# Optimization experiments

Hardware: AMD Instinct MI355X
Metric: run time of the kernel (lower is better)

## Reference

```python
import jax, jax.numpy as jnp
import numpy as np

EPS = 1e-5  # torch BatchNorm2d default


def _conv(x, w, padding):
    return jax.lax.conv_general_dilated(
        x, w, window_strides=(1, 1),
        padding=[(padding, padding), (padding, padding)],
        dimension_numbers=("NCHW", "OIHW", "NCHW"))


def _bn(x, gamma, beta):
    # training-mode batchnorm (biased variance), matching nn.BatchNorm2d forward
    mu = x.mean(axis=(0, 2, 3), keepdims=True)
    var = x.var(axis=(0, 2, 3), keepdims=True)
    xn = (x - mu) * jax.lax.rsqrt(var + EPS)
    return gamma[None, :, None, None] * xn + beta[None, :, None, None]


def _ste(x):
    # forward: sign(x); backward: pass gradient where |x| <= 1 (STE)
    m = (jnp.abs(x) <= 1.0).astype(x.dtype)
    s = jax.lax.stop_gradient(jnp.sign(x))
    return s + m * x - jax.lax.stop_gradient(m * x)


def _binconv(x, w, alpha, padding=1):
    # XNOR-style: sign both operands, full-precision conv, scale by alpha
    return _conv(jnp.sign(x), jnp.sign(w), padding) * alpha


def _maxpool2(x):
    return jax.lax.reduce_window(x, -jnp.inf, jax.lax.max,
                                 (1, 1, 2, 2), (1, 1, 2, 2), "VALID")


def setup_inputs() -> dict:
    key = jax.random.key(0)
    ks = jax.random.split(key, 8)

    def kaiming(k, shape):
        fan_out = shape[0] * shape[2] * shape[3]
        std = np.sqrt(2.0 / fan_out)
        return jax.random.normal(k, shape, dtype=jnp.float32) * std

    return {
        "x": jax.random.normal(ks[0], (128, 1, 128, 128), dtype=jnp.float32),
        # first conv (full precision) 1->32, k=3, pad=1
        "w1": kaiming(ks[1], (32, 1, 3, 3)),
        "b1": jnp.zeros((32,), jnp.float32),
        "g1": jnp.ones((32,), jnp.float32),
        "beta1": jnp.zeros((32,), jnp.float32),
        # BinaryConv2d 32->32
        "w2": kaiming(ks[2], (32, 32, 3, 3)),
        "a2": jnp.ones((1,), jnp.float32),
        "g2": jnp.ones((32,), jnp.float32),
        "beta2": jnp.zeros((32,), jnp.float32),
        # BinaryConv2d 32->64
        "w3": kaiming(ks[3], (64, 32, 3, 3)),
        "a3": jnp.ones((1,), jnp.float32),
        "g3": jnp.ones((64,), jnp.float32),
        "beta3": jnp.zeros((64,), jnp.float32),
        # BinaryConv2d 64->128
        "w4": kaiming(ks[4], (128, 64, 3, 3)),
        "a4": jnp.ones((1,), jnp.float32),
        # classifier 128->10
        "wf": jax.random.normal(ks[5], (10, 128), dtype=jnp.float32) * (1.0 / np.sqrt(128.0)),
        "bf": jnp.zeros((10,), jnp.float32),
    }


def reference(x, w1, b1, g1, beta1, w2, a2, g2, beta2, w3, a3, g3, beta3, w4, a4, wf, bf):
    h = _conv(x, w1, padding=1) + b1[None, :, None, None]   # [N,32,128,128]
    h = _bn(h, g1, beta1)
    h = _ste(h)
    h = _binconv(h, w2, a2)                                 # [N,32,128,128]
    h = _maxpool2(h)                                        # [N,32,64,64]
    h = _bn(h, g2, beta2)
    h = _ste(h)
    h = _binconv(h, w3, a3)                                 # [N,64,64,64]
    h = _maxpool2(h)                                        # [N,64,32,32]
    h = _bn(h, g3, beta3)
    h = _ste(h)
    h = _binconv(h, w4, a4)                                 # [N,128,32,32]
    h = h.mean(axis=(2, 3))                                 # AdaptiveAvgPool2d(1) -> [N,128]
    return h @ wf.T + bf                                    # [N,10]
```

## Files before the change

kernel.cpp:

```cpp
#include <hip/hip_runtime.h>
#include <stdint.h>
#include <limits.h>

constexpr int NB = 128;

__global__ void pack_weights_kernel(const float* __restrict__ w, uint32_t* __restrict__ out,
                                    int OC, int ICW)
{
    int idx = blockIdx.x * blockDim.x + threadIdx.x;
    int total = OC * 9 * ICW;
    if (idx >= total) return;
    int iw = idx % ICW;
    int t  = (idx / ICW) % 9;
    int oc = idx / (9 * ICW);
    int IC = ICW * 32;
    uint32_t word = 0;
    for (int b = 0; b < 32; ++b) {
        float wv = w[(size_t)(oc * IC + (iw * 32 + b)) * 9 + t];
        word |= (wv > 0.f ? 1u : 0u) << b;
    }
    out[idx] = word;
}

__device__ __forceinline__ void conv1_load9(const float* __restrict__ x, int p, float* xv)
{
    int n = p >> 14;
    int y = (p >> 7) & 127;
    int c = p & 127;
    const float* xn = x + (size_t)n * 16384;
    #pragma unroll
    for (int ky = 0; ky < 3; ++ky)
    #pragma unroll
    for (int kx = 0; kx < 3; ++kx) {
        int yy = y + ky - 1, cc = c + kx - 1;
        float v = 0.f;
        if (yy >= 0 && yy < 128 && cc >= 0 && cc < 128) v = xn[yy * 128 + cc];
        xv[ky * 3 + kx] = v;
    }
}

__global__ __launch_bounds__(256) void xcorr_kernel(const float* __restrict__ x,
                                                    float* __restrict__ partials)
{
    __shared__ float wbuf[4][64];
    int tid = threadIdx.x;
    float s[9], c[45];
    #pragma unroll
    for (int t = 0; t < 9; ++t) s[t] = 0.f;
    #pragma unroll
    for (int q = 0; q < 45; ++q) c[q] = 0.f;

    int base = blockIdx.x * 256 + tid;
    #pragma unroll 4
    for (int k = 0; k < 16; ++k) {
        float xv[9];
        conv1_load9(x, base + k * 131072, xv);
        #pragma unroll
        for (int t = 0; t < 9; ++t) {
            s[t] += xv[t];
            #pragma unroll
            for (int u = t; u < 9; ++u) {
                int q = t * (19 - t) / 2 + (u - t);
                c[q] = fmaf(xv[t], xv[u], c[q]);
            }
        }
    }
    #pragma unroll
    for (int t = 0; t < 9; ++t) {
        float a = s[t];
        #pragma unroll
        for (int off = 32; off >= 1; off >>= 1) a += __shfl_xor(a, off, 64);
        s[t] = a;
    }
    #pragma unroll
    for (int q = 0; q < 45; ++q) {
        float a = c[q];
        #pragma unroll
        for (int off = 32; off >= 1; off >>= 1) a += __shfl_xor(a, off, 64);
        c[q] = a;
    }
    int lane = tid & 63, wv = tid >> 6;
    if (lane == 0) {
        #pragma unroll
        for (int t = 0; t < 9; ++t) wbuf[wv][t] = s[t];
        #pragma unroll
        for (int q = 0; q < 45; ++q) wbuf[wv][9 + q] = c[q];
    }
    __syncthreads();
    if (tid < 54)
        partials[blockIdx.x * 64 + tid] =
            (wbuf[0][tid] + wbuf[1][tid]) + (wbuf[2][tid] + wbuf[3][tid]);
}

__global__ void compute_ss1_kernel(const double* __restrict__ dsums,
                                   const float* __restrict__ w1, const float* __restrict__ b1,
                                   const float* __restrict__ g1, const float* __restrict__ be1,
                                   float* __restrict__ ss)
{
    __shared__ double S[9], C[45];
    int tid = threadIdx.x;
    if (tid < 9) S[tid] = dsums[tid];
    else if (tid < 54) C[tid - 9] = dsums[tid];
    __syncthreads();
    if (tid >= 32) return;
    double b = (double)b1[tid];
    double w[9];
    #pragma unroll
    for (int t = 0; t < 9; ++t) w[t] = (double)w1[tid * 9 + t];
    double Sdot = 0.0, Q = 0.0;
    #pragma unroll
    for (int t = 0; t < 9; ++t) {
        Sdot += w[t] * S[t];
        #pragma unroll
        for (int u = t; u < 9; ++u) {
            int q = t * (19 - t) / 2 + (u - t);
            double term = w[t] * w[u] * C[q];
            Q += (u == t) ? term : 2.0 * term;
        }
    }
    const double N = 2097152.0;
    double mu  = Sdot / N + b;
    double ex2 = (Q + 2.0 * b * Sdot) / N + b * b;
    float var = (float)(ex2 - mu * mu);
    float A = g1[tid] * (1.f / sqrtf(var + 1e-5f));
    ss[tid] = A;
    ss[32 + tid] = be1[tid] - (float)mu * A;
}

__global__ __launch_bounds__(256) void conv1_pack_kernel(
    const float* __restrict__ x, const float* __restrict__ w1, const float* __restrict__ b1,
    const float* __restrict__ ss, uint32_t* __restrict__ s1)
{
    __shared__ float wl[384];
    int tid = threadIdx.x;
    for (int i = tid; i < 384; i += 256)
        wl[i] = (i < 288) ? w1[i] : ((i < 320) ? b1[i - 288] : ss[i - 320]);
    __syncthreads();

    float xv[4][9];
    int base = blockIdx.x * 256 + tid;
    #pragma unroll
    for (int i = 0; i < 4; ++i) conv1_load9(x, base + i * 524288, xv[i]);

    uint32_t word[4] = {0, 0, 0, 0};
    #pragma unroll
    for (int oc = 0; oc < 32; ++oc) {
        float w[9];
        #pragma unroll
        for (int t = 0; t < 9; ++t) w[t] = wl[oc * 9 + t];
        float b = wl[288 + oc];
        float A = wl[320 + oc], B = wl[352 + oc];
        #pragma unroll
        for (int i = 0; i < 4; ++i) {
            float a = b;
            #pragma unroll
            for (int t = 0; t < 9; ++t) a = fmaf(xv[i][t], w[t], a);
            float v = fmaf(A, a, B);
            word[i] |= (v > 0.f ? 1u : 0u) << oc;
        }
    }
    #pragma unroll
    for (int i = 0; i < 4; ++i) s1[base + i * 524288] = word[i];
}

template<int CH, int STRIDE>
__global__ __launch_bounds__(256) void reduce_partials_kernel(
    const float* __restrict__ partials, int nblk, double* __restrict__ dsums)
{
    __shared__ double wsum[4];
    int ch = blockIdx.x;
    int tid = threadIdx.x;
    double a = 0.0;
    for (int i = tid; i < nblk; i += 256)
        a += (double)partials[(size_t)i * STRIDE + ch];
    #pragma unroll
    for (int off = 32; off >= 1; off >>= 1)
        a += __shfl_xor(a, off, 64);
    if ((tid & 63) == 0) wsum[tid >> 6] = a;
    __syncthreads();
    if (tid == 0)
        dsums[ch] = (wsum[0] + wsum[1]) + (wsum[2] + wsum[3]);
}

template<int OC>
__global__ void compute_ss_kernel(const double* __restrict__ dsums,
                                  const float* __restrict__ gamma, const float* __restrict__ beta,
                                  float inv_n, float* __restrict__ ss)
{
    int tid = threadIdx.x;
    if (tid >= OC) return;
    float mu  = (float)dsums[tid] * inv_n;
    float ex2 = (float)dsums[OC + tid] * inv_n;
    float var = ex2 - mu * mu;
    float rs  = 1.f / sqrtf(var + 1e-5f);
    float A = gamma[tid] * rs;
    ss[tid] = A;
    ss[OC + tid] = beta[tid] - mu * A;
}

template<int W>
__device__ __forceinline__ void bc_load_window(const uint32_t* __restrict__ sin, int p,
                                               uint32_t* xw, uint32_t* wm, int* cnt)
{
    constexpr int PW = W / 2;
    int n = p / (PW * PW);
    int rem = p % (PW * PW);
    int py = rem / PW, px = rem % PW;
    int r0 = 2 * py - 1, c0 = 2 * px - 1;
    const uint32_t* sp = sin + (size_t)n * W * W;
    #pragma unroll
    for (int a = 0; a < 4; ++a) {
        int r = r0 + a;
        bool rv = (r >= 0) & (r < W);
        #pragma unroll
        for (int b = 0; b < 4; ++b) {
            int c = c0 + b;
            bool v = rv & (c >= 0) & (c < W);
            wm[a * 4 + b] = v ? 0xFFFFFFFFu : 0u;
            xw[a * 4 + b] = v ? sp[r * W + c] : 0u;
        }
    }
    #pragma unroll
    for (int a2 = 0; a2 < 2; ++a2)
    #pragma unroll
    for (int b2 = 0; b2 < 2; ++b2) {
        int cc = 0;
        #pragma unroll
        for (int ky = 0; ky < 3; ++ky)
        #pragma unroll
        for (int kx = 0; kx < 3; ++kx)
            cc += (int)(wm[(a2 + ky) * 4 + (b2 + kx)] & 1u);
        cnt[a2 * 2 + b2] = cc * 32;
    }
}

template<int OC, int W>
__global__ __launch_bounds__(256) void binconv_store_kernel(
    const uint32_t* __restrict__ sin, const uint32_t* __restrict__ wp,
    const float* __restrict__ alpha, float* __restrict__ partials,
    uint32_t* __restrict__ m16)
{
    constexpr int PW = W / 2;
    constexpr int TOTAL = NB * PW * PW;
    constexpr int G = 4;
    __shared__ uint32_t wl[OC * 9];
    __shared__ float wbuf[4][2 * OC];

    int tid = threadIdx.x;
    for (int i = tid; i < OC * 9; i += 256) wl[i] = wp[i];
    __syncthreads();
    float alp = alpha[0];
    bool useMax = (alp >= 0.f);
    int p = blockIdx.x * 256 + tid;

    uint32_t xw[16], wm[16];
    int cnt[4];
    bc_load_window<W>(sin, p, xw, wm, cnt);

    uint32_t packed[OC / 2];

    for (int g = 0; g < OC / G; ++g) {
        float s[G], s2[G];
        #pragma unroll
        for (int j = 0; j < G; ++j) {
            int oc = g * G + j;
            uint32_t w9[9];
            #pragma unroll
            for (int t = 0; t < 9; ++t) w9[t] = wl[oc * 9 + t];
            int mi = useMax ? INT_MIN : INT_MAX;
            #pragma unroll
            for (int a2 = 0; a2 < 2; ++a2)
            #pragma unroll
            for (int b2 = 0; b2 < 2; ++b2) {
                int pop = 0;
                #pragma unroll
                for (int ky = 0; ky < 3; ++ky)
                #pragma unroll
                for (int kx = 0; kx < 3; ++kx) {
                    int idx = (a2 + ky) * 4 + (b2 + kx);
                    pop += __popc((xw[idx] ^ w9[ky * 3 + kx]) & wm[idx]);
                }
                int vi = cnt[a2 * 2 + b2] - 2 * pop;
                mi = useMax ? max(mi, vi) : min(mi, vi);
            }
            float m = alp * (float)mi;
            s[j] = m; s2[j] = m * m;
            uint32_t h = (uint32_t)(uint16_t)(short)mi;
            if ((oc & 1) == 0) packed[oc >> 1] = h;
            else               packed[oc >> 1] |= h << 16;
        }
        int lane = tid & 63, wv = tid >> 6;
        #pragma unroll
        for (int j = 0; j < G; ++j) {
            float a = s[j], b = s2[j];
            #pragma unroll
            for (int off = 32; off >= 1; off >>= 1) {
                a += __shfl_xor(a, off, 64);
                b += __shfl_xor(b, off, 64);
            }
            if (lane == 0) { wbuf[wv][g * G + j] = a; wbuf[wv][OC + g * G + j] = b; }
        }
    }

    #pragma unroll
    for (int q = 0; q < OC / 2; ++q)
        m16[(size_t)q * TOTAL + p] = packed[q];

    __syncthreads();
    if (tid < 2 * OC)
        partials[blockIdx.x * (2 * OC) + tid] =
            (wbuf[0][tid] + wbuf[1][tid]) + (wbuf[2][tid] + wbuf[3][tid]);
}

template<int OC, int W>
__global__ __launch_bounds__(256) void binconv_pack_kernel(
    const uint32_t* __restrict__ m16, const float* __restrict__ alpha,
    const float* __restrict__ ss, void* __restrict__ sout)
{
    constexpr int PW = W / 2;
    constexpr int TOTAL = NB * PW * PW;
    __shared__ float Ap[OC], Bp[OC];
    int tid = threadIdx.x;
    if (tid < OC) { Ap[tid] = ss[tid] * alpha[0]; Bp[tid] = ss[OC + tid]; }
    __syncthreads();
    int p = blockIdx.x * 256 + tid;
    uint64_t word = 0;
    #pragma unroll
    for (int q = 0; q < OC / 2; ++q) {
        uint32_t u = m16[(size_t)q * TOTAL + p];
        int m0 = (int)(short)(u & 0xffffu);
        int m1 = (int)(short)(u >> 16);
        float v0 = fmaf(Ap[2 * q],     (float)m0, Bp[2 * q]);
        float v1 = fmaf(Ap[2 * q + 1], (float)m1, Bp[2 * q + 1]);
        word |= (v0 > 0.f ? 1ull : 0ull) << (2 * q);
        word |= (v1 > 0.f ? 1ull : 0ull) << (2 * q + 1);
    }
    if constexpr (OC == 32) ((uint32_t*)sout)[p] = (uint32_t)word;
    else                    ((uint64_t*)sout)[p] = word;
}

template<int OC, int W, int MODE, int G>
__global__ __launch_bounds__(256) void binconv_pool_kernel(
    const uint32_t* __restrict__ sin, const uint32_t* __restrict__ wp,
    const float* __restrict__ alpha, const float* __restrict__ ss,
    float* __restrict__ partials, void* __restrict__ sout)
{
    constexpr int PW = W / 2;
    __shared__ uint32_t wl[OC * 9];
    __shared__ float ssl[2 * OC];
    __shared__ float wbuf[4][2 * OC];

    int tid = threadIdx.x;
    for (int i = tid; i < OC * 9; i += 256) wl[i] = wp[i];
    if constexpr (MODE == 1) { if (tid < 2 * OC) ssl[tid] = ss[tid]; }
    __syncthreads();
    float alp = alpha[0];
    int p = blockIdx.x * 256 + tid;

    uint32_t xw[16], wm[16];
    int cnt[4];
    bc_load_window<W>(sin, p, xw, wm, cnt);

    uint64_t word = 0;
    for (int g = 0; g < OC / G; ++g) {
        float s[G], s2[G];
        #pragma unroll
        for (int j = 0; j < G; ++j) {
            int oc = g * G + j;
            uint32_t w9[9];
            #pragma unroll
            for (int t = 0; t < 9; ++t) w9[t] = wl[oc * 9 + t];
            float m = -3.4e38f;
            #pragma unroll
            for (int a2 = 0; a2 < 2; ++a2)
            #pragma unroll
            for (int b2 = 0; b2 < 2; ++b2) {
                int pop = 0;
                #pragma unroll
                for (int ky = 0; ky < 3; ++ky)
                #pragma unroll
                for (int kx = 0; kx < 3; ++kx) {
                    int idx = (a2 + ky) * 4 + (b2 + kx);
                    pop += __popc((xw[idx] ^ w9[ky * 3 + kx]) & wm[idx]);
                }
                float v = alp * (float)(cnt[a2 * 2 + b2] - 2 * pop);
                m = fmaxf(m, v);
            }
            if constexpr (MODE == 0) { s[j] = m; s2[j] = m * m; }
            else {
                float vv = fmaf(ssl[oc], m, ssl[OC + oc]);
                word |= (vv > 0.f ? 1ull : 0ull) << oc;
            }
        }
        if constexpr (MODE == 0) {
            int lane = tid & 63, wv = tid >> 6;
            #pragma unroll
            for (int j = 0; j < G; ++j) {
                float a = s[j], b = s2[j];
                #pragma unroll
                for (int off = 32; off >= 1; off >>= 1) {
                    a += __shfl_xor(a, off, 64);
                    b += __shfl_xor(b, off, 64);
                }
                if (lane == 0) { wbuf[wv][g * G + j] = a; wbuf[wv][OC + g * G + j] = b; }
            }
        }
    }

    if constexpr (MODE == 1) {
        if constexpr (OC == 32) ((uint32_t*)sout)[p] = (uint32_t)word;
        else                    ((uint64_t*)sout)[p] = word;
    } else {
        __syncthreads();
        if (tid < 2 * OC)
            partials[blockIdx.x * (2 * OC) + tid] =
                (wbuf[0][tid] + wbuf[1][tid]) + (wbuf[2][tid] + wbuf[3][tid]);
    }
}

__global__ __launch_bounds__(256) void conv4_partial_kernel(
    const uint64_t* __restrict__ s3, const uint64_t* __restrict__ wp4,
    float* __restrict__ p4)
{
    __shared__ uint64_t xt[192];
    __shared__ uint64_t wl[1152];
    __shared__ float red[256];
    int b = blockIdx.x;
    int n = b >> 3, s = b & 7;
    int tid = threadIdx.x;
    for (int i = tid; i < 192; i += 256) {
        int row = 4 * s - 1 + (i >> 5);
        int col = i & 31;
        xt[i] = (row >= 0 && row < 32) ? s3[(size_t)n * 1024 + row * 32 + col] : 0ull;
    }
    for (int i = tid; i < 1152; i += 256) wl[i] = wp4[i];
    __syncthreads();
    int oc = tid & 127, h = tid >> 7;
    uint64_t wr[9];
    #pragma unroll
    for (int t = 0; t < 9; ++t) wr[t] = wl[oc * 9 + t];
    int acc = 0;
    #pragma unroll
    for (int ry = 0; ry < 2; ++ry) {
        int lry = 2 * h + ry;
        int y = 4 * s + lry;
        for (int x = 0; x < 32; ++x) {
            int pop = 0, c = 0;
            #pragma unroll
            for (int ky = 0; ky < 3; ++ky) {
                int yy = y + ky - 1;
                if (yy < 0 || yy >= 32) continue;
                int lrow = lry + ky;
                #pragma unroll
                for (int kx = 0; kx < 3; ++kx) {
                    int xx = x + kx - 1;
                    if (xx < 0 || xx >= 32) continue;
                    pop += __popcll(xt[lrow * 32 + xx] ^ wr[ky * 3 + kx]);
                    c += 64;
                }
            }
            acc += c - 2 * pop;
        }
    }
    red[tid] = (float)acc;
    __syncthreads();
    if (tid < 128)
        p4[(size_t)b * 128 + tid] = red[tid] + red[tid + 128];
}

__global__ void mean4_kernel(const float* __restrict__ p4, const float* __restrict__ alpha4,
                             float* __restrict__ mean4)
{
    int t = blockIdx.x * blockDim.x + threadIdx.x;
    if (t >= NB * 128) return;
    int n = t >> 7, oc = t & 127;
    float a = 0.f;
    #pragma unroll
    for (int s = 0; s < 8; ++s)
        a += p4[(size_t)((n * 8 + s) * 128) + oc];
    mean4[t] = a * alpha4[0] * (1.f / 1024.f);
}

__global__ void linear_kernel(const float* __restrict__ mean4, const float* __restrict__ wf,
                              const float* __restrict__ bf, float* __restrict__ out)
{
    int t = blockIdx.x * blockDim.x + threadIdx.x;
    if (t >= 1280) return;
    int n = t / 10, k = t % 10;
    const float* m = mean4 + n * 128;
    const float* w = wf + k * 128;
    float a = bf[k];
    #pragma unroll 4
    for (int i = 0; i < 128; ++i) a = fmaf(m[i], w[i], a);
    out[t] = a;
}

extern "C" void kernel_launch(void* const* d_in, const int* in_sizes, int n_in,
                              void* d_out, int out_size, void* d_ws, size_t ws_size,
                              hipStream_t stream)
{
    const float* x   = (const float*)d_in[0];
    const float* w1  = (const float*)d_in[1];
    const float* b1  = (const float*)d_in[2];
    const float* g1  = (const float*)d_in[3];
    const float* be1 = (const float*)d_in[4];
    const float* w2  = (const float*)d_in[5];
    const float* a2  = (const float*)d_in[6];
    const float* g2  = (const float*)d_in[7];
    const float* be2 = (const float*)d_in[8];
    const float* w3  = (const float*)d_in[9];
    const float* a3  = (const float*)d_in[10];
    const float* g3  = (const float*)d_in[11];
    const float* be3 = (const float*)d_in[12];
    const float* w4  = (const float*)d_in[13];
    const float* a4  = (const float*)d_in[14];
    const float* wf  = (const float*)d_in[15];
    const float* bf  = (const float*)d_in[16];
    float* out = (float*)d_out;

    uint8_t* ws = (uint8_t*)d_ws;
    size_t off = 0;
    auto alloc = [&](size_t bytes) -> void* {
        void* p = ws + off;
        off += (bytes + 255) & ~(size_t)255;
        return p;
    };
    uint32_t* wp2 = (uint32_t*)alloc(288 * 4);
    uint32_t* wp3 = (uint32_t*)alloc(576 * 4);
    uint32_t* wp4 = (uint32_t*)alloc(2304 * 4);
    float* ss1 = (float*)alloc(64 * 4);
    float* ss2 = (float*)alloc(64 * 4);
    float* ss3 = (float*)alloc(128 * 4);
    double* dsums = (double*)alloc(128 * 8);
    uint32_t* s1 = (uint32_t*)alloc((size_t)128 * 128 * 128 * 4);
    uint32_t* s2 = (uint32_t*)alloc((size_t)128 * 64 * 64 * 4);
    uint64_t* s3 = (uint64_t*)alloc((size_t)128 * 32 * 32 * 8);
    float* mean4 = (float*)alloc((size_t)128 * 128 * 4);
    float* p4    = (float*)alloc((size_t)1024 * 128 * 4);
    float* partials = (float*)alloc((size_t)2048 * 64 * 4);
    size_t base_off = off;
    uint32_t* m16_2 = (uint32_t*)alloc((size_t)16 * 524288 * 4);
    uint32_t* m16_3 = (uint32_t*)alloc((size_t)32 * 131072 * 4);
    bool fused = (off <= ws_size);
    (void)base_off;

    pack_weights_kernel<<<2, 256, 0, stream>>>(w2, wp2, 32, 1);
    pack_weights_kernel<<<3, 256, 0, stream>>>(w3, wp3, 64, 1);
    pack_weights_kernel<<<9, 256, 0, stream>>>(w4, wp4, 128, 2);

    xcorr_kernel<<<512, 256, 0, stream>>>(x, partials);
    reduce_partials_kernel<54, 64><<<54, 256, 0, stream>>>(partials, 512, dsums);
    compute_ss1_kernel<<<1, 64, 0, stream>>>(dsums, w1, b1, g1, be1, ss1);
    conv1_pack_kernel<<<2048, 256, 0, stream>>>(x, w1, b1, ss1, s1);

    if (fused) {
        binconv_store_kernel<32, 128><<<2048, 256, 0, stream>>>(s1, wp2, a2, partials, m16_2);
        reduce_partials_kernel<64, 64><<<64, 256, 0, stream>>>(partials, 2048, dsums);
        compute_ss_kernel<32><<<1, 32, 0, stream>>>(dsums, g2, be2, 1.f / 524288.f, ss2);
        binconv_pack_kernel<32, 128><<<2048, 256, 0, stream>>>(m16_2, a2, ss2, (void*)s2);

        binconv_store_kernel<64, 64><<<512, 256, 0, stream>>>(s2, wp3, a3, partials, m16_3);
        reduce_partials_kernel<128, 128><<<128, 256, 0, stream>>>(partials, 512, dsums);
        compute_ss_kernel<64><<<1, 64, 0, stream>>>(dsums, g3, be3, 1.f / 131072.f, ss3);
        binconv_pack_kernel<64, 64><<<512, 256, 0, stream>>>(m16_3, a3, ss3, (void*)s3);
    } else {
        binconv_pool_kernel<32, 128, 0, 4><<<2048, 256, 0, stream>>>(s1, wp2, a2, nullptr, partials, nullptr);
        reduce_partials_kernel<64, 64><<<64, 256, 0, stream>>>(partials, 2048, dsums);
        compute_ss_kernel<32><<<1, 32, 0, stream>>>(dsums, g2, be2, 1.f / 524288.f, ss2);
        binconv_pool_kernel<32, 128, 1, 4><<<2048, 256, 0, stream>>>(s1, wp2, a2, ss2, nullptr, (void*)s2);

        binconv_pool_kernel<64, 64, 0, 4><<<512, 256, 0, stream>>>(s2, wp3, a3, nullptr, partials, nullptr);
        reduce_partials_kernel<128, 128><<<128, 256, 0, stream>>>(partials, 512, dsums);
        compute_ss_kernel<64><<<1, 64, 0, stream>>>(dsums, g3, be3, 1.f / 131072.f, ss3);
        binconv_pool_kernel<64, 64, 1, 4><<<512, 256, 0, stream>>>(s2, wp3, a3, ss3, nullptr, (void*)s3);
    }

    conv4_partial_kernel<<<1024, 256, 0, stream>>>(s3, (const uint64_t*)wp4, p4);
    mean4_kernel<<<64, 256, 0, stream>>>(p4, a4, mean4);
    linear_kernel<<<5, 256, 0, stream>>>(mean4, wf, bf, out);
}
```

Before: 244.7 us.

## Use zero-padded sign maps with branchless interior binconv, border fixup and separate stats

```diff
diff --git a/kernel.cpp b/kernel.cpp
--- a/kernel.cpp
+++ b/kernel.cpp
@@ -22,6 +22,13 @@
     out[idx] = word;
 }
 
+__global__ void zero_kernel(uint32_t* __restrict__ p, int n)
+{
+    int i = blockIdx.x * blockDim.x + threadIdx.x;
+    int stride = gridDim.x * blockDim.x;
+    for (; i < n; i += stride) p[i] = 0u;
+}
+
 __device__ __forceinline__ void conv1_load9(const float* __restrict__ x, int p, float* xv)
 {
     int n = p >> 14;
@@ -127,42 +134,6 @@
     ss[32 + tid] = be1[tid] - (float)mu * A;
 }
 
-__global__ __launch_bounds__(256) void conv1_pack_kernel(
-    const float* __restrict__ x, const float* __restrict__ w1, const float* __restrict__ b1,
-    const float* __restrict__ ss, uint32_t* __restrict__ s1)
-{
-    __shared__ float wl[384];
-    int tid = threadIdx.x;
-    for (int i = tid; i < 384; i += 256)
-        wl[i] = (i < 288) ? w1[i] : ((i < 320) ? b1[i - 288] : ss[i - 320]);
-    __syncthreads();
-
-    float xv[4][9];
-    int base = blockIdx.x * 256 + tid;
-    #pragma unroll
-    for (int i = 0; i < 4; ++i) conv1_load9(x, base + i * 524288, xv[i]);
-
-    uint32_t word[4] = {0, 0, 0, 0};
-    #pragma unroll
-    for (int oc = 0; oc < 32; ++oc) {
-        float w[9];
-        #pragma unroll
-        for (int t = 0; t < 9; ++t) w[t] = wl[oc * 9 + t];
-        float b = wl[288 + oc];
-        float A = wl[320 + oc], B = wl[352 + oc];
-        #pragma unroll
-        for (int i = 0; i < 4; ++i) {
-            float a = b;
-            #pragma unroll
-            for (int t = 0; t < 9; ++t) a = fmaf(xv[i][t], w[t], a);
-            float v = fmaf(A, a, B);
-            word[i] |= (v > 0.f ? 1u : 0u) << oc;
-        }
-    }
-    #pragma unroll
-    for (int i = 0; i < 4; ++i) s1[base + i * 524288] = word[i];
-}
-
 template<int CH, int STRIDE>
 __global__ __launch_bounds__(256) void reduce_partials_kernel(
     const float* __restrict__ partials, int nblk, double* __restrict__ dsums)
@@ -182,44 +153,133 @@
         dsums[ch] = (wsum[0] + wsum[1]) + (wsum[2] + wsum[3]);
 }
 
-template<int OC>
-__global__ void compute_ss_kernel(const double* __restrict__ dsums,
-                                  const float* __restrict__ gamma, const float* __restrict__ beta,
-                                  float inv_n, float* __restrict__ ss)
-{
-    int tid = threadIdx.x;
-    if (tid >= OC) return;
-    float mu  = (float)dsums[tid] * inv_n;
-    float ex2 = (float)dsums[OC + tid] * inv_n;
-    float var = ex2 - mu * mu;
-    float rs  = 1.f / sqrtf(var + 1e-5f);
-    float A = gamma[tid] * rs;
-    ss[tid] = A;
-    ss[OC + tid] = beta[tid] - mu * A;
-}
-
-template<int W>
-__device__ __forceinline__ void bc_load_window(const uint32_t* __restrict__ sin, int p,
-                                               uint32_t* xw, uint32_t* wm, int* cnt)
-{
-    constexpr int PW = W / 2;
-    int n = p / (PW * PW);
-    int rem = p % (PW * PW);
-    int py = rem / PW, px = rem % PW;
-    int r0 = 2 * py - 1, c0 = 2 * px - 1;
-    const uint32_t* sp = sin + (size_t)n * W * W;
+__global__ __launch_bounds__(256) void conv1_pack2_kernel(
+    const float* __restrict__ x, const float* __restrict__ w1, const float* __restrict__ b1,
+    const float* __restrict__ ss, uint32_t* __restrict__ s1p)
+{
+    __shared__ float wl[32 * 12];
+    __shared__ float abl[64];
+    int tid = threadIdx.x;
+    for (int i = tid; i < 288; i += 256) wl[(i / 9) * 12 + (i % 9)] = w1[i];
+    if (tid < 32) {
+        float A = ss[tid];
+        abl[2 * tid] = A;
+        abl[2 * tid + 1] = fmaf(A, b1[tid], ss[32 + tid]);
+    }
+    __syncthreads();
+    int p = blockIdx.x * 256 + tid;
+    float xv[9];
+    conv1_load9(x, p, xv);
+    int n = p >> 14, y = (p >> 7) & 127, c = p & 127;
+
+    uint32_t word = 0;
+    for (int oc = 0; oc < 32; ++oc) {
+        float4 wa = *(const float4*)&wl[oc * 12];
+        float4 wb = *(const float4*)&wl[oc * 12 + 4];
+        float w8 = wl[oc * 12 + 8];
+        float2 ab = *(const float2*)&abl[oc * 2];
+        float a = xv[0] * wa.x;
+        a = fmaf(xv[1], wa.y, a);
+        a = fmaf(xv[2], wa.z, a);
+        a = fmaf(xv[3], wa.w, a);
+        a = fmaf(xv[4], wb.x, a);
+        a = fmaf(xv[5], wb.y, a);
+        a = fmaf(xv[6], wb.z, a);
+        a = fmaf(xv[7], wb.w, a);
+        a = fmaf(xv[8], w8, a);
+        float v = fmaf(ab.x, a, ab.y);
+        word |= (v > 0.f ? 1u : 0u) << oc;
+    }
+    s1p[(size_t)n * 16900 + (y + 1) * 130 + (c + 1)] = word;
+}
+
+template<int OC, int PW, int LPW>
+__global__ __launch_bounds__(256) void binconv_main_kernel(
+    const uint32_t* __restrict__ sp_in, const uint32_t* __restrict__ wp,
+    const float* __restrict__ alpha, uint32_t* __restrict__ m16)
+{
+    constexpr int PS = 2 * PW + 2;
+    constexpr int TOTAL = NB * PW * PW;
+    __shared__ uint32_t wl[OC * 12];
+    int tid = threadIdx.x;
+    for (int i = tid; i < OC * 9; i += 256) wl[(i / 9) * 12 + (i % 9)] = wp[i];
+    __syncthreads();
+    bool useMax = (alpha[0] >= 0.f);
+    int p = blockIdx.x * 256 + tid;
+    int px = p & (PW - 1), py = (p >> LPW) & (PW - 1), n = p >> (2 * LPW);
+    const uint32_t* base = sp_in + (size_t)n * PS * PS + (2 * py) * PS + 2 * px;
+
+    uint32_t xw[16];
+    #pragma unroll
+    for (int r = 0; r < 4; ++r) {
+        uint2 a = *(const uint2*)(base + r * PS);
+        uint2 b = *(const uint2*)(base + r * PS + 2);
+        xw[r * 4 + 0] = a.x; xw[r * 4 + 1] = a.y;
+        xw[r * 4 + 2] = b.x; xw[r * 4 + 3] = b.y;
+    }
+
+    uint32_t pend = 0;
+    for (int oc = 0; oc < OC; ++oc) {
+        uint4 wa = *(const uint4*)&wl[oc * 12];
+        uint4 wb = *(const uint4*)&wl[oc * 12 + 4];
+        uint32_t w8 = wl[oc * 12 + 8];
+        uint32_t w[9] = {wa.x, wa.y, wa.z, wa.w, wb.x, wb.y, wb.z, wb.w, w8};
+        int s0 = 0, s1 = 0, s2 = 0, s3 = 0;
+        #pragma unroll
+        for (int ky = 0; ky < 3; ++ky)
+        #pragma unroll
+        for (int kx = 0; kx < 3; ++kx) {
+            uint32_t wt = w[ky * 3 + kx];
+            s0 += __popc(xw[ky * 4 + kx]           ^ wt);
+            s1 += __popc(xw[ky * 4 + kx + 1]       ^ wt);
+            s2 += __popc(xw[(ky + 1) * 4 + kx]     ^ wt);
+            s3 += __popc(xw[(ky + 1) * 4 + kx + 1] ^ wt);
+        }
+        int sm = useMax ? min(min(s0, s1), min(s2, s3))
+                        : max(max(s0, s1), max(s2, s3));
+        int m = 288 - 2 * sm;
+        if ((oc & 1) == 0) pend = (uint32_t)(uint16_t)(short)m;
+        else m16[(size_t)(oc >> 1) * TOTAL + p] = pend | ((uint32_t)(uint16_t)(short)m << 16);
+    }
+}
+
+template<int OC, int PW>
+__global__ __launch_bounds__(256) void binconv_fix_kernel(
+    const uint32_t* __restrict__ sp_in, const uint32_t* __restrict__ wp,
+    const float* __restrict__ alpha, uint32_t* __restrict__ m16)
+{
+    constexpr int PS = 2 * PW + 2;
+    constexpr int TOTAL = NB * PW * PW;
+    constexpr int RING = 4 * PW - 4;
+    __shared__ uint32_t wl[OC * 12];
+    int tid = threadIdx.x;
+    for (int i = tid; i < OC * 9; i += 256) wl[(i / 9) * 12 + (i % 9)] = wp[i];
+    __syncthreads();
+    bool useMax = (alpha[0] >= 0.f);
+    int t = blockIdx.x * 256 + tid;
+    int n = t / RING, r = t % RING;
+    int py, px;
+    if (r < PW)              { py = 0;      px = r; }
+    else if (r < 2 * PW)     { py = PW - 1; px = r - PW; }
+    else if (r < 3 * PW - 2) { px = 0;      py = r - 2 * PW + 1; }
+    else                     { px = PW - 1; py = r - (3 * PW - 2) + 1; }
+    int p = n * PW * PW + py * PW + px;
+    const uint32_t* base = sp_in + (size_t)n * PS * PS + (2 * py) * PS + 2 * px;
+
+    uint32_t xw[16], wm[16];
     #pragma unroll
     for (int a = 0; a < 4; ++a) {
-        int r = r0 + a;
-        bool rv = (r >= 0) & (r < W);
+        int rr = 2 * py - 1 + a;
+        bool rv = (rr >= 0) && (rr < 2 * PW);
         #pragma unroll
         for (int b = 0; b < 4; ++b) {
-            int c = c0 + b;
-            bool v = rv & (c >= 0) & (c < W);
+            int cc = 2 * px - 1 + b;
+            bool v = rv && (cc >= 0) && (cc < 2 * PW);
             wm[a * 4 + b] = v ? 0xFFFFFFFFu : 0u;
-            xw[a * 4 + b] = v ? sp[r * W + c] : 0u;
+            xw[a * 4 + b] = base[a * PS + b];
         }
     }
+    int cnt[4];
     #pragma unroll
     for (int a2 = 0; a2 < 2; ++a2)
     #pragma unroll
@@ -232,92 +292,104 @@
             cc += (int)(wm[(a2 + ky) * 4 + (b2 + kx)] & 1u);
         cnt[a2 * 2 + b2] = cc * 32;
     }
-}
-
-template<int OC, int W>
-__global__ __launch_bounds__(256) void binconv_store_kernel(
-    const uint32_t* __restrict__ sin, const uint32_t* __restrict__ wp,
-    const float* __restrict__ alpha, float* __restrict__ partials,
-    uint32_t* __restrict__ m16)
-{
-    constexpr int PW = W / 2;
-    constexpr int TOTAL = NB * PW * PW;
-    constexpr int G = 4;
-    __shared__ uint32_t wl[OC * 9];
-    __shared__ float wbuf[4][2 * OC];
-
-    int tid = threadIdx.x;
-    for (int i = tid; i < OC * 9; i += 256) wl[i] = wp[i];
-    __syncthreads();
-    float alp = alpha[0];
-    bool useMax = (alp >= 0.f);
-    int p = blockIdx.x * 256 + tid;
-
-    uint32_t xw[16], wm[16];
-    int cnt[4];
-    bc_load_window<W>(sin, p, xw, wm, cnt);
-
-    uint32_t packed[OC / 2];
-
-    for (int g = 0; g < OC / G; ++g) {
-        float s[G], s2[G];
-        #pragma unroll
-        for (int j = 0; j < G; ++j) {
-            int oc = g * G + j;
-            uint32_t w9[9];
+
+    uint32_t pend = 0;
+    for (int oc = 0; oc < OC; ++oc) {
+        uint4 wa = *(const uint4*)&wl[oc * 12];
+        uint4 wb = *(const uint4*)&wl[oc * 12 + 4];
+        uint32_t w8 = wl[oc * 12 + 8];
+        uint32_t w[9] = {wa.x, wa.y, wa.z, wa.w, wb.x, wb.y, wb.z, wb.w, w8};
+        int v[4];
+        #pragma unroll
+        for (int a2 = 0; a2 < 2; ++a2)
+        #pragma unroll
+        for (int b2 = 0; b2 < 2; ++b2) {
+            int pop = 0;
             #pragma unroll
-            for (int t = 0; t < 9; ++t) w9[t] = wl[oc * 9 + t];
-            int mi = useMax ? INT_MIN : INT_MAX;
+            for (int ky = 0; ky < 3; ++ky)
             #pragma unroll
-            for (int a2 = 0; a2 < 2; ++a2)
-            #pragma unroll
-            for (int b2 = 0; b2 < 2; ++b2) {
-                int pop = 0;
-                #pragma unroll
-                for (int ky = 0; ky < 3; ++ky)
-                #pragma unroll
-                for (int kx = 0; kx < 3; ++kx) {
-                    int idx = (a2 + ky) * 4 + (b2 + kx);
-                    pop += __popc((xw[idx] ^ w9[ky * 3 + kx]) & wm[idx]);
-                }
-                int vi = cnt[a2 * 2 + b2] - 2 * pop;
-                mi = useMax ? max(mi, vi) : min(mi, vi);
+            for (int kx = 0; kx < 3; ++kx) {
+                int idx = (a2 + ky) * 4 + (b2 + kx);
+                pop += __popc((xw[idx] ^ w[ky * 3 + kx]) & wm[idx]);
             }
-            float m = alp * (float)mi;
-            s[j] = m; s2[j] = m * m;
-            uint32_t h = (uint32_t)(uint16_t)(short)mi;
-            if ((oc & 1) == 0) packed[oc >> 1] = h;
-            else               packed[oc >> 1] |= h << 16;
+            v[a2 * 2 + b2] = cnt[a2 * 2 + b2] - 2 * pop;
         }
-        int lane = tid & 63, wv = tid >> 6;
-        #pragma unroll
-        for (int j = 0; j < G; ++j) {
-            float a = s[j], b = s2[j];
-            #pragma unroll
-            for (int off = 32; off >= 1; off >>= 1) {
-                a += __shfl_xor(a, off, 64);
-                b += __shfl_xor(b, off, 64);
-            }
-            if (lane == 0) { wbuf[wv][g * G + j] = a; wbuf[wv][OC + g * G + j] = b; }
-        }
-    }
-
-    #pragma unroll
-    for (int q = 0; q < OC / 2; ++q)
-        m16[(size_t)q * TOTAL + p] = packed[q];
-
-    __syncthreads();
-    if (tid < 2 * OC)
-        partials[blockIdx.x * (2 * OC) + tid] =
-            (wbuf[0][tid] + wbuf[1][tid]) + (wbuf[2][tid] + wbuf[3][tid]);
-}
-
-template<int OC, int W>
+        int m = useMax ? max(max(v[0], v[1]), max(v[2], v[3]))
+                       : min(min(v[0], v[1]), min(v[2], v[3]));
+        if ((oc & 1) == 0) pend = (uint32_t)(uint16_t)(short)m;
+        else m16[(size_t)(oc >> 1) * TOTAL + p] = pend | ((uint32_t)(uint16_t)(short)m << 16);
+    }
+}
+
+template<int PIXELS, int CHUNKS>
+__global__ __launch_bounds__(256) void stats16_kernel(const uint32_t* __restrict__ m16,
+                                                      double* __restrict__ pd)
+{
+    __shared__ int wb[4][4];
+    int bid = blockIdx.x;
+    int q = bid / CHUNKS, ch = bid % CHUNKS;
+    const uint32_t* pl = m16 + (size_t)q * PIXELS + (size_t)ch * (PIXELS / CHUNKS);
+    int tid = threadIdx.x;
+    int s0 = 0, s1 = 0, q0 = 0, q1 = 0;
+    #pragma unroll 4
+    for (int j = 0; j < PIXELS / CHUNKS / 256; ++j) {
+        uint32_t u = pl[tid + j * 256];
+        int m0 = (int)(short)(u & 0xffffu);
+        int m1 = (int)u >> 16;
+        s0 += m0; s1 += m1;
+        q0 += m0 * m0; q1 += m1 * m1;
+    }
+    #pragma unroll
+    for (int off = 32; off >= 1; off >>= 1) {
+        s0 += __shfl_xor(s0, off, 64); s1 += __shfl_xor(s1, off, 64);
+        q0 += __shfl_xor(q0, off, 64); q1 += __shfl_xor(q1, off, 64);
+    }
+    int lane = tid & 63, w = tid >> 6;
+    if (lane == 0) { wb[w][0] = s0; wb[w][1] = s1; wb[w][2] = q0; wb[w][3] = q1; }
+    __syncthreads();
+    if (tid < 4)
+        pd[(size_t)bid * 4 + tid] =
+            (double)((long long)wb[0][tid] + wb[1][tid] + wb[2][tid] + wb[3][tid]);
+}
+
+template<int OC, int CHUNKS>
+__global__ void reduce_stats16_kernel(const double* __restrict__ pd, double* __restrict__ dsums)
+{
+    int ch = blockIdx.x;
+    bool issq = ch >= OC;
+    int c = issq ? ch - OC : ch;
+    int q = c >> 1;
+    int slot = (issq ? 2 : 0) + (c & 1);
+    int tid = threadIdx.x;
+    double a = (tid < CHUNKS) ? pd[(size_t)(q * CHUNKS + tid) * 4 + slot] : 0.0;
+    #pragma unroll
+    for (int off = 32; off >= 1; off >>= 1)
+        a += __shfl_xor(a, off, 64);
+    if (tid == 0) dsums[ch] = a;
+}
+
+template<int OC>
+__global__ void compute_ss_alpha_kernel(const double* __restrict__ dsums,
+                                        const float* __restrict__ gamma, const float* __restrict__ beta,
+                                        const float* __restrict__ alpha,
+                                        float inv_n, float* __restrict__ ss)
+{
+    int tid = threadIdx.x;
+    if (tid >= OC) return;
+    double al = (double)alpha[0];
+    float mu  = (float)(dsums[tid] * al * (double)inv_n);
+    float ex2 = (float)(dsums[OC + tid] * al * al * (double)inv_n);
+    float var = ex2 - mu * mu;
+    float A = gamma[tid] * (1.f / sqrtf(var + 1e-5f));
+    ss[tid] = A;
+    ss[OC + tid] = beta[tid] - mu * A;
+}
+
+template<int OC, int PW, int LPW, bool PADOUT>
 __global__ __launch_bounds__(256) void binconv_pack_kernel(
     const uint32_t* __restrict__ m16, const float* __restrict__ alpha,
     const float* __restrict__ ss, void* __restrict__ sout)
 {
-    constexpr int PW = W / 2;
     constexpr int TOTAL = NB * PW * PW;
     __shared__ float Ap[OC], Bp[OC];
     int tid = threadIdx.x;
@@ -329,92 +401,18 @@
     for (int q = 0; q < OC / 2; ++q) {
         uint32_t u = m16[(size_t)q * TOTAL + p];
         int m0 = (int)(short)(u & 0xffffu);
-        int m1 = (int)(short)(u >> 16);
+        int m1 = (int)u >> 16;
         float v0 = fmaf(Ap[2 * q],     (float)m0, Bp[2 * q]);
         float v1 = fmaf(Ap[2 * q + 1], (float)m1, Bp[2 * q + 1]);
         word |= (v0 > 0.f ? 1ull : 0ull) << (2 * q);
         word |= (v1 > 0.f ? 1ull : 0ull) << (2 * q + 1);
     }
-    if constexpr (OC == 32) ((uint32_t*)sout)[p] = (uint32_t)word;
-    else                    ((uint64_t*)sout)[p] = word;
-}
-
-template<int OC, int W, int MODE, int G>
-__global__ __launch_bounds__(256) void binconv_pool_kernel(
-    const uint32_t* __restrict__ sin, const uint32_t* __restrict__ wp,
-    const float* __restrict__ alpha, const float* __restrict__ ss,
-    float* __restrict__ partials, void* __restrict__ sout)
-{
-    constexpr int PW = W / 2;
-    __shared__ uint32_t wl[OC * 9];
-    __shared__ float ssl[2 * OC];
-    __shared__ float wbuf[4][2 * OC];
-
-    int tid = threadIdx.x;
-    for (int i = tid; i < OC * 9; i += 256) wl[i] = wp[i];
-    if constexpr (MODE == 1) { if (tid < 2 * OC) ssl[tid] = ss[tid]; }
-    __syncthreads();
-    float alp = alpha[0];
-    int p = blockIdx.x * 256 + tid;
-
-    uint32_t xw[16], wm[16];
-    int cnt[4];
-    bc_load_window<W>(sin, p, xw, wm, cnt);
-
-    uint64_t word = 0;
-    for (int g = 0; g < OC / G; ++g) {
-        float s[G], s2[G];
-        #pragma unroll
-        for (int j = 0; j < G; ++j) {
-            int oc = g * G + j;
-            uint32_t w9[9];
-            #pragma unroll
-            for (int t = 0; t < 9; ++t) w9[t] = wl[oc * 9 + t];
-            float m = -3.4e38f;
-            #pragma unroll
-            for (int a2 = 0; a2 < 2; ++a2)
-            #pragma unroll
-            for (int b2 = 0; b2 < 2; ++b2) {
-                int pop = 0;
-                #pragma unroll
-                for (int ky = 0; ky < 3; ++ky)
-                #pragma unroll
-                for (int kx = 0; kx < 3; ++kx) {
-                    int idx = (a2 + ky) * 4 + (b2 + kx);
-                    pop += __popc((xw[idx] ^ w9[ky * 3 + kx]) & wm[idx]);
-                }
-                float v = alp * (float)(cnt[a2 * 2 + b2] - 2 * pop);
-                m = fmaxf(m, v);
-            }
-            if constexpr (MODE == 0) { s[j] = m; s2[j] = m * m; }
-            else {
-                float vv = fmaf(ssl[oc], m, ssl[OC + oc]);
-                word |= (vv > 0.f ? 1ull : 0ull) << oc;
-            }
-        }
-        if constexpr (MODE == 0) {
-            int lane = tid & 63, wv = tid >> 6;
-            #pragma unroll
-            for (int j = 0; j < G; ++j) {
-                float a = s[j], b = s2[j];
-                #pragma unroll
-                for (int off = 32; off >= 1; off >>= 1) {
-                    a += __shfl_xor(a, off, 64);
-                    b += __shfl_xor(b, off, 64);
-                }
-                if (lane == 0) { wbuf[wv][g * G + j] = a; wbuf[wv][OC + g * G + j] = b; }
-            }
-        }
-    }
-
-    if constexpr (MODE == 1) {
-        if constexpr (OC == 32) ((uint32_t*)sout)[p] = (uint32_t)word;
-        else                    ((uint64_t*)sout)[p] = word;
+    if constexpr (PADOUT) {
+        int px = p & (PW - 1), py = (p >> LPW) & (PW - 1), n = p >> (2 * LPW);
+        ((uint32_t*)sout)[(size_t)n * (PW + 2) * (PW + 2) + (py + 1) * (PW + 2) + (px + 1)]
+            = (uint32_t)word;
     } else {
-        __syncthreads();
-        if (tid < 2 * OC)
-            partials[blockIdx.x * (2 * OC) + tid] =
-                (wbuf[0][tid] + wbuf[1][tid]) + (wbuf[2][tid] + wbuf[3][tid]);
+        ((uint64_t*)sout)[p] = word;
     }
 }
 
@@ -531,18 +529,19 @@
     float* ss1 = (float*)alloc(64 * 4);
     float* ss2 = (float*)alloc(64 * 4);
     float* ss3 = (float*)alloc(128 * 4);
-    double* dsums = (double*)alloc(128 * 8);
-    uint32_t* s1 = (uint32_t*)alloc((size_t)128 * 128 * 128 * 4);
-    uint32_t* s2 = (uint32_t*)alloc((size_t)128 * 64 * 64 * 4);
-    uint64_t* s3 = (uint64_t*)alloc((size_t)128 * 32 * 32 * 8);
+    double* dsums = (double*)alloc(256 * 8);
+    double* pd    = (double*)alloc(2048 * 8);
+    float* partials = (float*)alloc((size_t)512 * 64 * 4);
+    uint32_t* s1p = (uint32_t*)alloc((size_t)128 * 16900 * 4);
+    uint32_t* s2p = (uint32_t*)alloc((size_t)128 * 4356 * 4);
+    uint64_t* s3  = (uint64_t*)alloc((size_t)128 * 1024 * 8);
     float* mean4 = (float*)alloc((size_t)128 * 128 * 4);
     float* p4    = (float*)alloc((size_t)1024 * 128 * 4);
-    float* partials = (float*)alloc((size_t)2048 * 64 * 4);
-    size_t base_off = off;
     uint32_t* m16_2 = (uint32_t*)alloc((size_t)16 * 524288 * 4);
     uint32_t* m16_3 = (uint32_t*)alloc((size_t)32 * 131072 * 4);
-    bool fused = (off <= ws_size);
-    (void)base_off;
+
+    zero_kernel<<<2048, 256, 0, stream>>>(s1p, 128 * 16900);
+    zero_kernel<<<1024, 256, 0, stream>>>(s2p, 128 * 4356);
 
     pack_weights_kernel<<<2, 256, 0, stream>>>(w2, wp2, 32, 1);
     pack_weights_kernel<<<3, 256, 0, stream>>>(w3, wp3, 64, 1);
@@ -551,29 +550,21 @@
     xcorr_kernel<<<512, 256, 0, stream>>>(x, partials);
     reduce_partials_kernel<54, 64><<<54, 256, 0, stream>>>(partials, 512, dsums);
     compute_ss1_kernel<<<1, 64, 0, stream>>>(dsums, w1, b1, g1, be1, ss1);
-    conv1_pack_kernel<<<2048, 256, 0, stream>>>(x, w1, b1, ss1, s1);
-
-    if (fused) {
-        binconv_store_kernel<32, 128><<<2048, 256, 0, stream>>>(s1, wp2, a2, partials, m16_2);
-        reduce_partials_kernel<64, 64><<<64, 256, 0, stream>>>(partials, 2048, dsums);
-        compute_ss_kernel<32><<<1, 32, 0, stream>>>(dsums, g2, be2, 1.f / 524288.f, ss2);
-        binconv_pack_kernel<32, 128><<<2048, 256, 0, stream>>>(m16_2, a2, ss2, (void*)s2);
-
-        binconv_store_kernel<64, 64><<<512, 256, 0, stream>>>(s2, wp3, a3, partials, m16_3);
-        reduce_partials_kernel<128, 128><<<128, 256, 0, stream>>>(partials, 512, dsums);
-        compute_ss_kernel<64><<<1, 64, 0, stream>>>(dsums, g3, be3, 1.f / 131072.f, ss3);
-        binconv_pack_kernel<64, 64><<<512, 256, 0, stream>>>(m16_3, a3, ss3, (void*)s3);
-    } else {
-        binconv_pool_kernel<32, 128, 0, 4><<<2048, 256, 0, stream>>>(s1, wp2, a2, nullptr, partials, nullptr);
-        reduce_partials_kernel<64, 64><<<64, 256, 0, stream>>>(partials, 2048, dsums);
-        compute_ss_kernel<32><<<1, 32, 0, stream>>>(dsums, g2, be2, 1.f / 524288.f, ss2);
-        binconv_pool_kernel<32, 128, 1, 4><<<2048, 256, 0, stream>>>(s1, wp2, a2, ss2, nullptr, (void*)s2);
-
-        binconv_pool_kernel<64, 64, 0, 4><<<512, 256, 0, stream>>>(s2, wp3, a3, nullptr, partials, nullptr);
-        reduce_partials_kernel<128, 128><<<128, 256, 0, stream>>>(partials, 512, dsums);
-        compute_ss_kernel<64><<<1, 64, 0, stream>>>(dsums, g3, be3, 1.f / 131072.f, ss3);
-        binconv_pool_kernel<64, 64, 1, 4><<<512, 256, 0, stream>>>(s2, wp3, a3, ss3, nullptr, (void*)s3);
-    }
+    conv1_pack2_kernel<<<8192, 256, 0, stream>>>(x, w1, b1, ss1, s1p);
+
+    binconv_main_kernel<32, 64, 6><<<2048, 256, 0, stream>>>(s1p, wp2, a2, m16_2);
+    binconv_fix_kernel<32, 64><<<126, 256, 0, stream>>>(s1p, wp2, a2, m16_2);
+    stats16_kernel<524288, 32><<<512, 256, 0, stream>>>(m16_2, pd);
+    reduce_stats16_kernel<32, 32><<<64, 64, 0, stream>>>(pd, dsums);
+    compute_ss_alpha_kernel<32><<<1, 32, 0, stream>>>(dsums, g2, be2, a2, 1.f / 524288.f, ss2);
+    binconv_pack_kernel<32, 64, 6, true><<<2048, 256, 0, stream>>>(m16_2, a2, ss2, (void*)s2p);
+
+    binconv_main_kernel<64, 32, 5><<<512, 256, 0, stream>>>(s2p, wp3, a3, m16_3);
+    binconv_fix_kernel<64, 32><<<62, 256, 0, stream>>>(s2p, wp3, a3, m16_3);
+    stats16_kernel<131072, 8><<<256, 256, 0, stream>>>(m16_3, pd);
+    reduce_stats16_kernel<64, 8><<<128, 64, 0, stream>>>(pd, dsums);
+    compute_ss_alpha_kernel<64><<<1, 64, 0, stream>>>(dsums, g3, be3, a3, 1.f / 131072.f, ss3);
+    binconv_pack_kernel<64, 32, 5, false><<<512, 256, 0, stream>>>(m16_3, a3, ss3, (void*)s3);
 
     conv4_partial_kernel<<<1024, 256, 0, stream>>>(s3, (const uint64_t*)wp4, p4);
     mean4_kernel<<<64, 256, 0, stream>>>(p4, a4, mean4);
```

Measured after the change: 261.8 us. 1.07x slower.
